# Performance work log

Measured on AMD Instinct MI355X. Metric: run time of the kernel, lower is better.

Reference implementation:

```python
import jax, jax.numpy as jnp
import numpy as np

B, S, T = 32, 64, 64          # batch, src_len, tgt_len
E, H, V = 512, 1024, 32000    # embed, hidden, vocab
WSCALE = 0.05                 # keep tanh/sigmoid in sane range


def setup_inputs() -> dict:
    key = jax.random.key(0)
    ks = jax.random.split(key, 14)
    n = lambda k, shp: jax.random.normal(k, shp, jnp.float32)
    return {
        "target": jax.random.randint(ks[0], (B, T), 0, V),
        "src_enc": n(ks[1], (B, S, 2 * H)),
        "h0": n(ks[2], (B, H)),
        "c0": n(ks[3], (B, H)),
        "emb": n(ks[4], (V, E)) * WSCALE,
        "W_ih": n(ks[5], (E, 4 * H)) * WSCALE,
        "W_hh": n(ks[6], (H, 4 * H)) * WSCALE,
        "b_rnn": jnp.zeros((4 * H,), jnp.float32),
        "W_attn": n(ks[7], (2 * H, H)) * WSCALE,
        "b_attn": jnp.zeros((H,), jnp.float32),
        "W_comb": n(ks[8], (2 * H, H)) * WSCALE,
        "b_comb": jnp.zeros((H,), jnp.float32),
        "W_out": n(ks[9], (H, V)) * WSCALE,
        "b_out": jnp.zeros((V,), jnp.float32),
    }


def reference(target, src_enc, h0, c0, emb, W_ih, W_hh, b_rnn,
              W_attn, b_attn, W_comb, b_comb, W_out, b_out):
    # Pre-project encoder states once (decode() applies attention.linear up front)
    enc_proj = src_enc @ W_attn + b_attn                 # [B,S,H]
    xs = emb[target[:, :-1]]                             # teacher forcing [B,T-1,E]
    xs = jnp.swapaxes(xs, 0, 1)                          # [T-1,B,E] for scan

    def step(carry, x_t):
        h, c = carry
        # LSTM cell (torch gate order i, f, g, o)
        gates = x_t @ W_ih + h @ W_hh + b_rnn            # [B,4H]
        i, f, g, o = jnp.split(gates, 4, axis=-1)
        c = jax.nn.sigmoid(f) * c + jax.nn.sigmoid(i) * jnp.tanh(g)
        h = jax.nn.sigmoid(o) * jnp.tanh(c)
        # Bilinear attention: score = h^T (W_attn e_s) over source positions
        scores = jnp.einsum('bsh,bh->bs', enc_proj, h)
        attn = jax.nn.softmax(scores, axis=-1)
        ctx = jnp.einsum('bs,bsh->bh', attn, enc_proj)   # [B,H]
        out = jnp.tanh(jnp.concatenate([h, ctx], axis=-1) @ W_comb + b_comb)
        return (h, c), out

    _, outs = jax.lax.scan(step, (h0, c0), xs)           # [T-1,B,H]
    outs = jnp.swapaxes(outs, 0, 1)                      # [B,T-1,H]
    logits = outs @ W_out + b_out                        # [B,T-1,V]
    return logits
```

## Files before the change

### kernel.cpp

```cpp
#include <hip/hip_runtime.h>
#include <stdint.h>

#define NB    32
#define NS    64
#define TDEC  63
#define NE    512
#define NH    1024
#define NV    32000

typedef float  floatx4 __attribute__((ext_vector_type(4)));
typedef short  short8  __attribute__((ext_vector_type(8)));
typedef short  short4v __attribute__((ext_vector_type(4)));

__device__ __forceinline__ float bf2f(short s) {
  return __uint_as_float(((uint32_t)(uint16_t)s) << 16);
}
__device__ __forceinline__ short f2bf(float f) {
  uint32_t u = __float_as_uint(f);
  uint32_t r = (u + 0x7fffu + ((u >> 16) & 1u)) >> 16;
  return (short)(uint16_t)r;
}
__device__ __forceinline__ float sigm(float x) { return 1.f / (1.f + expf(-x)); }

template<int PERM>
__global__ __launch_bounds__(256) void transpose_bf(
    const float* __restrict__ W, short* __restrict__ Wt, int K, int N)
{
  __shared__ float tile[32][33];
  int k0 = blockIdx.x * 32, n0 = blockIdx.y * 32;
  int tx = threadIdx.x & 31, ty = threadIdx.x >> 5;
#pragma unroll
  for (int r = 0; r < 32; r += 8)
    tile[ty + r][tx] = W[(size_t)(k0 + ty + r) * N + n0 + tx];
  __syncthreads();
  int kq = threadIdx.x & 7, nl = threadIdx.x >> 3;
  int n = n0 + nl;
  int rr = PERM ? ((n & 1023) * 4 + (n >> 10)) : n;
  short4v v;
#pragma unroll
  for (int q = 0; q < 4; ++q) v[q] = f2bf(tile[kq * 4 + q][nl]);
  *(short4v*)&Wt[(size_t)rr * K + k0 + kq * 4] = v;
}

template<int PERM>
__global__ __launch_bounds__(256) void transpose_bf_split(
    const float* __restrict__ W, short* __restrict__ Wt_hi,
    short* __restrict__ Wt_lo, int K, int N)
{
  __shared__ float tile[32][33];
  int k0 = blockIdx.x * 32, n0 = blockIdx.y * 32;
  int tx = threadIdx.x & 31, ty = threadIdx.x >> 5;
#pragma unroll
  for (int r = 0; r < 32; r += 8)
    tile[ty + r][tx] = W[(size_t)(k0 + ty + r) * N + n0 + tx];
  __syncthreads();
  int kq = threadIdx.x & 7, nl = threadIdx.x >> 3;
  int n = n0 + nl;
  int rr = PERM ? ((n & 1023) * 4 + (n >> 10)) : n;
  short4v vh, vl;
#pragma unroll
  for (int q = 0; q < 4; ++q) {
    float v = tile[kq * 4 + q][nl];
    short h = f2bf(v);
    vh[q] = h;
    vl[q] = f2bf(v - bf2f(h));
  }
  size_t o = (size_t)rr * K + k0 + kq * 4;
  *(short4v*)&Wt_hi[o] = vh;
  *(short4v*)&Wt_lo[o] = vl;
}

__global__ __launch_bounds__(256) void gather_init(
    const int* __restrict__ target, const float* __restrict__ emb,
    const float* __restrict__ h0, const float* __restrict__ c0,
    const float* __restrict__ brnn,
    short* __restrict__ xs, float* __restrict__ hf_ring,
    short* __restrict__ hhi_ring, short* __restrict__ hlo_ring,
    float* __restrict__ c_buf, float* __restrict__ brnn_p)
{
  const int NXS = TDEC * NB * NE;
  const int HN = NH * NB;
  int total = NXS + 2 * HN + 4096;
  for (int idx = blockIdx.x * 256 + threadIdx.x; idx < total; idx += gridDim.x * 256) {
    if (idx < NXS) {
      int row = idx >> 9, e = idx & 511;
      int t = row >> 5, b = row & 31;
      int token = target[b * 64 + t];
      xs[idx] = f2bf(emb[(size_t)token * NE + e]);
    } else if (idx < NXS + HN) {
      int r = idx - NXS;
      float v = h0[r];
      hf_ring[r] = v;
      short hh = f2bf(v);
      hhi_ring[r] = hh;
      hlo_ring[r] = f2bf(v - bf2f(hh));
    } else if (idx < NXS + 2 * HN) {
      int r = idx - NXS - HN;
      c_buf[r] = c0[r];
    } else {
      int c = idx - NXS - 2 * HN;
      brnn_p[c] = brnn[(c & 3) * 1024 + (c >> 2)];
    }
  }
}

template<int OUT_BF>
__global__ __launch_bounds__(256) void gemm_kernel(
    const short* __restrict__ Ab, const short* __restrict__ Bt,
    void* __restrict__ Cptr, const float* __restrict__ bias,
    int M, int N, int K)
{
  __shared__ short As[128 * 40];
  __shared__ short Bs[128 * 40];
  __shared__ float cst[OUT_BF ? 1 : 32 * 132];
  const int m0 = blockIdx.x * 128;
  const int n0 = blockIdx.y * 128;
  const int tid = threadIdx.x;
  const int lane = tid & 63;
  const int wid = tid >> 6;
  const int wr = wid >> 1, wc = wid & 1;

  floatx4 acc[4][4] = {};
  const int row = tid >> 1;
  const int kh  = (tid & 1) << 4;

  for (int k0 = 0; k0 < K; k0 += 32) {
    {
      int gm = m0 + row;
      short8 lo, hi;
      if (gm < M) {
        const short* src = Ab + (size_t)gm * K + k0 + kh;
        lo = *(const short8*)src;
        hi = *(const short8*)(src + 8);
      } else {
#pragma unroll
        for (int c = 0; c < 8; ++c) { lo[c] = 0; hi[c] = 0; }
      }
      *(short8*)&As[row * 40 + kh]     = lo;
      *(short8*)&As[row * 40 + kh + 8] = hi;
    }
    {
      const short* src = Bt + (size_t)(n0 + row) * K + k0 + kh;
      *(short8*)&Bs[row * 40 + kh]     = *(const short8*)src;
      *(short8*)&Bs[row * 40 + kh + 8] = *(const short8*)(src + 8);
    }
    __syncthreads();

    const int kA = (lane >> 4) << 3;
    const int rsel = lane & 15;
    short8 af[4], bfr[4];
#pragma unroll
    for (int mi = 0; mi < 4; ++mi)
      af[mi] = *(const short8*)&As[(wr * 64 + mi * 16 + rsel) * 40 + kA];
#pragma unroll
    for (int ni = 0; ni < 4; ++ni)
      bfr[ni] = *(const short8*)&Bs[(wc * 64 + ni * 16 + rsel) * 40 + kA];
#pragma unroll
    for (int mi = 0; mi < 4; ++mi)
#pragma unroll
      for (int ni = 0; ni < 4; ++ni)
        acc[mi][ni] = __builtin_amdgcn_mfma_f32_16x16x32_bf16(af[mi], bfr[ni], acc[mi][ni], 0, 0, 0);
    __syncthreads();
  }

  const int crow = (lane >> 4) * 4;
  const int ccol = lane & 15;
  if (OUT_BF) {
#pragma unroll
    for (int mi = 0; mi < 4; ++mi) {
#pragma unroll
      for (int ni = 0; ni < 4; ++ni) {
        int gn = n0 + wc * 64 + ni * 16 + ccol;
        float bv = bias[gn];
#pragma unroll
        for (int i = 0; i < 4; ++i) {
          int gm = m0 + wr * 64 + mi * 16 + crow + i;
          if (gm < M)
            ((short*)Cptr)[(size_t)gm * N + gn] = f2bf(acc[mi][ni][i] + bv);
        }
      }
    }
  } else {
#pragma unroll
    for (int p = 0; p < 4; ++p) {
      __syncthreads();
      if (wr == (p >> 1)) {
        int mi0 = (p & 1) * 2;
#pragma unroll
        for (int mm = 0; mm < 2; ++mm) {
#pragma unroll
          for (int ni = 0; ni < 4; ++ni) {
            int c = wc * 64 + ni * 16 + ccol;
#pragma unroll
            for (int i = 0; i < 4; ++i)
              cst[(mm * 16 + crow + i) * 132 + c] = acc[mi0 + mm][ni][i];
          }
        }
      }
      __syncthreads();
#pragma unroll
      for (int rep = 0; rep < 4; ++rep) {
        int cell = tid + rep * 256;
        int r = cell >> 5, q = cell & 31;
        int gm = m0 + p * 32 + r;
        int gn = n0 + q * 4;
        if (gm < M) {
          float4 bv = *(const float4*)&bias[gn];
          float4 v;
          v.x = cst[r * 132 + q * 4 + 0] + bv.x;
          v.y = cst[r * 132 + q * 4 + 1] + bv.y;
          v.z = cst[r * 132 + q * 4 + 2] + bv.z;
          v.w = cst[r * 132 + q * 4 + 3] + bv.w;
          *(float4*)&((float*)Cptr)[(size_t)gm * N + gn] = v;
        }
      }
    }
  }
}

__global__ __launch_bounds__(256) void gemm_split(
    const float* __restrict__ A, const short* __restrict__ Bt_hi,
    const short* __restrict__ Bt_lo, float* __restrict__ C,
    const float* __restrict__ bias, int M, int N, int K)
{
  __shared__ short As_hi[128 * 40];
  __shared__ short As_lo[128 * 40];
  __shared__ short Bs_hi[128 * 40];
  __shared__ short Bs_lo[128 * 40];
  const int m0 = blockIdx.x * 128;
  const int n0 = blockIdx.y * 128;
  const int tid = threadIdx.x;
  const int lane = tid & 63;
  const int wid = tid >> 6;
  const int wr = wid >> 1, wc = wid & 1;

  floatx4 acc[4][4] = {};
  const int row = tid >> 1;
  const int kh  = (tid & 1) << 4;

  for (int k0 = 0; k0 < K; k0 += 32) {
    {
      const float* src = A + (size_t)(m0 + row) * K + k0 + kh;
      short8 h0v, h1, l0, l1;
#pragma unroll
      for (int c = 0; c < 8; ++c) {
        float v = src[c];
        short h = f2bf(v); h0v[c] = h; l0[c] = f2bf(v - bf2f(h));
        float w = src[c + 8];
        short g = f2bf(w); h1[c] = g; l1[c] = f2bf(w - bf2f(g));
      }
      *(short8*)&As_hi[row * 40 + kh]     = h0v;
      *(short8*)&As_hi[row * 40 + kh + 8] = h1;
      *(short8*)&As_lo[row * 40 + kh]     = l0;
      *(short8*)&As_lo[row * 40 + kh + 8] = l1;
    }
    {
      size_t o = (size_t)(n0 + row) * K + k0 + kh;
      *(short8*)&Bs_hi[row * 40 + kh]     = *(const short8*)(Bt_hi + o);
      *(short8*)&Bs_hi[row * 40 + kh + 8] = *(const short8*)(Bt_hi + o + 8);
      *(short8*)&Bs_lo[row * 40 + kh]     = *(const short8*)(Bt_lo + o);
      *(short8*)&Bs_lo[row * 40 + kh + 8] = *(const short8*)(Bt_lo + o + 8);
    }
    __syncthreads();

    const int kA = (lane >> 4) << 3;
    const int rsel = lane & 15;
    short8 ah[4], al[4], bh[4], bl[4];
#pragma unroll
    for (int mi = 0; mi < 4; ++mi) {
      int off = (wr * 64 + mi * 16 + rsel) * 40 + kA;
      ah[mi] = *(const short8*)&As_hi[off];
      al[mi] = *(const short8*)&As_lo[off];
    }
#pragma unroll
    for (int ni = 0; ni < 4; ++ni) {
      int off = (wc * 64 + ni * 16 + rsel) * 40 + kA;
      bh[ni] = *(const short8*)&Bs_hi[off];
      bl[ni] = *(const short8*)&Bs_lo[off];
    }
#pragma unroll
    for (int mi = 0; mi < 4; ++mi)
#pragma unroll
      for (int ni = 0; ni < 4; ++ni) {
        floatx4 a = acc[mi][ni];
        a = __builtin_amdgcn_mfma_f32_16x16x32_bf16(al[mi], bh[ni], a, 0, 0, 0);
        a = __builtin_amdgcn_mfma_f32_16x16x32_bf16(ah[mi], bl[ni], a, 0, 0, 0);
        a = __builtin_amdgcn_mfma_f32_16x16x32_bf16(ah[mi], bh[ni], a, 0, 0, 0);
        acc[mi][ni] = a;
      }
    __syncthreads();
  }

  const int crow = (lane >> 4) * 4;
  const int ccol = lane & 15;
#pragma unroll
  for (int mi = 0; mi < 4; ++mi) {
#pragma unroll
    for (int ni = 0; ni < 4; ++ni) {
      int gn = n0 + wc * 64 + ni * 16 + ccol;
      float bv = bias[gn];
#pragma unroll
      for (int i = 0; i < 4; ++i) {
        int gm = m0 + wr * 64 + mi * 16 + crow + i;
        C[(size_t)gm * N + gn] = acc[mi][ni][i] + bv;
      }
    }
  }
}

__global__ __launch_bounds__(512) void scan_step(
    int iter,
    const short* __restrict__ Whp_hi,
    const short* __restrict__ Whp_lo,
    const short* __restrict__ WcT_hi,
    const short* __restrict__ WcT_lo,
    const float* __restrict__ bcomb,
    const float* __restrict__ encp,
    const short* __restrict__ gatesx,
    short* __restrict__ hhi_ring,
    short* __restrict__ hlo_ring,
    float* __restrict__ hf_ring,
    short* __restrict__ ctxhi_ring,
    short* __restrict__ ctxlo_ring,
    float* __restrict__ c_buf,
    short* __restrict__ outs)
{
  __shared__ float smem[8 * 32 * 33];
  const int blk = blockIdx.x;
  const int tid = threadIdx.x;
  const int lane = tid & 63;
  const int wid = tid >> 6;
  const int rsel = lane & 15;
  const int kA = (lane >> 4) * 8;
  const int crow = (lane >> 4) * 4;
  const int ccol = lane & 15;

  if (blk < 128) {
    const int t = iter;
    if (t >= TDEC) return;
    const size_t spv = (size_t)(t & 3) * (NH * NB);
    const size_t snw = (size_t)((t + 1) & 3) * (NH * NB);
    const short* Hh = hhi_ring + spv;
    const short* Hl = hlo_ring + spv;
    const int c0 = blk * 32;
    const int kb = wid * 128;

    floatx4 acc[2][2] = {};
    const short* wh0 = Whp_hi + (size_t)(c0 + rsel) * NH + kb + kA;
    const short* wl0 = Whp_lo + (size_t)(c0 + rsel) * NH + kb + kA;
    const short* wh1 = Whp_hi + (size_t)(c0 + 16 + rsel) * NH + kb + kA;
    const short* wl1 = Whp_lo + (size_t)(c0 + 16 + rsel) * NH + kb + kA;
    const short* ha0 = Hh + (size_t)rsel * NH + kb + kA;
    const short* la0 = Hl + (size_t)rsel * NH + kb + kA;
    const short* ha1 = Hh + (size_t)(16 + rsel) * NH + kb + kA;
    const short* la1 = Hl + (size_t)(16 + rsel) * NH + kb + kA;
#pragma unroll
    for (int kk = 0; kk < 4; ++kk) {
      int k0 = kk * 32;
      short8 a0h = *(const short8*)(ha0 + k0);
      short8 a0l = *(const short8*)(la0 + k0);
      short8 a1h = *(const short8*)(ha1 + k0);
      short8 a1l = *(const short8*)(la1 + k0);
      short8 b0h = *(const short8*)(wh0 + k0);
      short8 b0l = *(const short8*)(wl0 + k0);
      short8 b1h = *(const short8*)(wh1 + k0);
      short8 b1l = *(const short8*)(wl1 + k0);
      acc[0][0] = __builtin_amdgcn_mfma_f32_16x16x32_bf16(a0l, b0h, acc[0][0], 0, 0, 0);
      acc[0][0] = __builtin_amdgcn_mfma_f32_16x16x32_bf16(a0h, b0l, acc[0][0], 0, 0, 0);
      acc[0][0] = __builtin_amdgcn_mfma_f32_16x16x32_bf16(a0h, b0h, acc[0][0], 0, 0, 0);
      acc[0][1] = __builtin_amdgcn_mfma_f32_16x16x32_bf16(a0l, b1h, acc[0][1], 0, 0, 0);
      acc[0][1] = __builtin_amdgcn_mfma_f32_16x16x32_bf16(a0h, b1l, acc[0][1], 0, 0, 0);
      acc[0][1] = __builtin_amdgcn_mfma_f32_16x16x32_bf16(a0h, b1h, acc[0][1], 0, 0, 0);
      acc[1][0] = __builtin_amdgcn_mfma_f32_16x16x32_bf16(a1l, b0h, acc[1][0], 0, 0, 0);
      acc[1][0] = __builtin_amdgcn_mfma_f32_16x16x32_bf16(a1h, b0l, acc[1][0], 0, 0, 0);
      acc[1][0] = __builtin_amdgcn_mfma_f32_16x16x32_bf16(a1h, b0h, acc[1][0], 0, 0, 0);
      acc[1][1] = __builtin_amdgcn_mfma_f32_16x16x32_bf16(a1l, b1h, acc[1][1], 0, 0, 0);
      acc[1][1] = __builtin_amdgcn_mfma_f32_16x16x32_bf16(a1h, b1l, acc[1][1], 0, 0, 0);
      acc[1][1] = __builtin_amdgcn_mfma_f32_16x16x32_bf16(a1h, b1h, acc[1][1], 0, 0, 0);
    }
#pragma unroll
    for (int mi = 0; mi < 2; ++mi)
#pragma unroll
      for (int ni = 0; ni < 2; ++ni)
#pragma unroll
        for (int i = 0; i < 4; ++i)
          smem[wid * 1056 + (mi * 16 + crow + i) * 33 + ni * 16 + ccol] = acc[mi][ni][i];
    __syncthreads();
    if (tid < 256) {
      int b = tid & 31, jl = tid >> 5;
      float g[4];
#pragma unroll
      for (int q = 0; q < 4; ++q) {
        float s = 0;
#pragma unroll
        for (int w = 0; w < 8; ++w) s += smem[w * 1056 + b * 33 + jl * 4 + q];
        g[q] = s;
      }
      int jg = (c0 >> 2) + jl;
      const short* gx = gatesx + ((size_t)t * 32 + b) * 4096 + c0 + jl * 4;
      short4v gxv = *(const short4v*)gx;
      float gi = g[0] + bf2f(gxv[0]);
      float gf = g[1] + bf2f(gxv[1]);
      float gg = g[2] + bf2f(gxv[2]);
      float go = g[3] + bf2f(gxv[3]);
      float co = c_buf[b * NH + jg];
      float cn = sigm(gf) * co + sigm(gi) * tanhf(gg);
      float hn = sigm(go) * tanhf(cn);
      c_buf[b * NH + jg] = cn;
      hf_ring[snw + b * NH + jg] = hn;
      short hh = f2bf(hn);
      hhi_ring[snw + b * NH + jg] = hh;
      hlo_ring[snw + b * NH + jg] = f2bf(hn - bf2f(hh));
    }
  } else if (blk < 160) {
    const int t = iter - 1;
    if (t < 0 || t >= TDEC) return;
    const int b = blk - 128;
    const float* h = hf_ring + (size_t)((t + 1) & 3) * (NH * NB) + b * NH;
    const size_t cslot = (size_t)(t & 1) * (NH * NB) + b * NH;
    short* ctxh = ctxhi_ring + cslot;
    short* ctxl = ctxlo_ring + cslot;
    float* h_lds  = smem;
    float* sc_lds = smem + 1024;
    float* p_lds  = smem + 1088;
    if (tid < 256) {
      float4 v = ((const float4*)h)[tid];
      ((float4*)h_lds)[tid] = v;
    }
    __syncthreads();
    {
      const float4* hl4 = (const float4*)(h_lds + lane * 16);
      float4 hv0 = hl4[0], hv1 = hl4[1], hv2 = hl4[2], hv3 = hl4[3];
      for (int si = 0; si < 8; ++si) {
        int s = wid * 8 + si;
        const float4* ep = (const float4*)(encp + ((size_t)(b * 64 + s)) * NH + lane * 16);
        float4 e0 = ep[0], e1 = ep[1], e2 = ep[2], e3 = ep[3];
        float a = e0.x * hv0.x + e0.y * hv0.y + e0.z * hv0.z + e0.w * hv0.w;
        a = fmaf(e1.x, hv1.x, a); a = fmaf(e1.y, hv1.y, a);
        a = fmaf(e1.z, hv1.z, a); a = fmaf(e1.w, hv1.w, a);
        a = fmaf(e2.x, hv2.x, a); a = fmaf(e2.y, hv2.y, a);
        a = fmaf(e2.z, hv2.z, a); a = fmaf(e2.w, hv2.w, a);
        a = fmaf(e3.x, hv3.x, a); a = fmaf(e3.y, hv3.y, a);
        a = fmaf(e3.z, hv3.z, a); a = fmaf(e3.w, hv3.w, a);
#pragma unroll
        for (int off = 32; off; off >>= 1) a += __shfl_xor(a, off);
        if (lane == 0) sc_lds[s] = a;
      }
    }
    __syncthreads();
    if (tid < 64) {
      float sc = sc_lds[tid];
      float m = sc;
#pragma unroll
      for (int off = 32; off; off >>= 1) m = fmaxf(m, __shfl_xor(m, off));
      float e = expf(sc - m);
      float sum = e;
#pragma unroll
      for (int off = 32; off; off >>= 1) sum += __shfl_xor(sum, off);
      p_lds[tid] = e / sum;
    }
    __syncthreads();
    if (tid < 256) {
      int k4 = tid * 4;
      float a0 = 0, a1 = 0, a2 = 0, a3 = 0;
      const float* ep = encp + (size_t)(b * 64) * NH + k4;
      for (int s = 0; s < 64; ++s) {
        float p = p_lds[s];
        float4 e = *(const float4*)(ep + (size_t)s * NH);
        a0 = fmaf(p, e.x, a0); a1 = fmaf(p, e.y, a1);
        a2 = fmaf(p, e.z, a2); a3 = fmaf(p, e.w, a3);
      }
      short4v c4h, c4l;
      float av[4] = {a0, a1, a2, a3};
#pragma unroll
      for (int q = 0; q < 4; ++q) {
        short hh = f2bf(av[q]);
        c4h[q] = hh;
        c4l[q] = f2bf(av[q] - bf2f(hh));
      }
      *(short4v*)(ctxh + k4) = c4h;
      *(short4v*)(ctxl + k4) = c4l;
    }
  } else {
    const int t = iter - 2;
    if (t < 0) return;
    const int j0 = (blk - 160) * 16;
    const size_t hslot = (size_t)((t + 1) & 3) * (NH * NB);
    const size_t cslot = (size_t)(t & 1) * (NH * NB);
    const short* Ah = (wid < 4) ? (hhi_ring + hslot) : (ctxhi_ring + cslot);
    const short* Al = (wid < 4) ? (hlo_ring + hslot) : (ctxlo_ring + cslot);
    const int kb = (wid & 3) * 256;
    const int kabs = wid * 256;

    floatx4 acc[2] = {};
    const short* bhp = WcT_hi + (size_t)(j0 + rsel) * 2048 + kabs + kA;
    const short* blp = WcT_lo + (size_t)(j0 + rsel) * 2048 + kabs + kA;
    const short* a0hp = Ah + (size_t)rsel * NH + kb + kA;
    const short* a0lp = Al + (size_t)rsel * NH + kb + kA;
    const short* a1hp = Ah + (size_t)(16 + rsel) * NH + kb + kA;
    const short* a1lp = Al + (size_t)(16 + rsel) * NH + kb + kA;
#pragma unroll
    for (int kk = 0; kk < 8; ++kk) {
      int k0 = kk * 32;
      short8 a0h = *(const short8*)(a0hp + k0);
      short8 a0l = *(const short8*)(a0lp + k0);
      short8 a1h = *(const short8*)(a1hp + k0);
      short8 a1l = *(const short8*)(a1lp + k0);
      short8 b_h = *(const short8*)(bhp + k0);
      short8 b_l = *(const short8*)(blp + k0);
      acc[0] = __builtin_amdgcn_mfma_f32_16x16x32_bf16(a0l, b_h, acc[0], 0, 0, 0);
      acc[0] = __builtin_amdgcn_mfma_f32_16x16x32_bf16(a0h, b_l, acc[0], 0, 0, 0);
      acc[0] = __builtin_amdgcn_mfma_f32_16x16x32_bf16(a0h, b_h, acc[0], 0, 0, 0);
      acc[1] = __builtin_amdgcn_mfma_f32_16x16x32_bf16(a1l, b_h, acc[1], 0, 0, 0);
      acc[1] = __builtin_amdgcn_mfma_f32_16x16x32_bf16(a1h, b_l, acc[1], 0, 0, 0);
      acc[1] = __builtin_amdgcn_mfma_f32_16x16x32_bf16(a1h, b_h, acc[1], 0, 0, 0);
    }
#pragma unroll
    for (int mi = 0; mi < 2; ++mi)
#pragma unroll
      for (int i = 0; i < 4; ++i)
        smem[wid * 544 + (mi * 16 + crow + i) * 17 + ccol] = acc[mi][i];
    __syncthreads();
    {
      int b = tid & 31, jl = tid >> 5;
      float s = 0;
#pragma unroll
      for (int w = 0; w < 8; ++w) s += smem[w * 544 + b * 17 + jl];
      float v = tanhf(s + bcomb[j0 + jl]);
      outs[((size_t)b * TDEC + t) * NH + j0 + jl] = f2bf(v);
    }
  }
}

extern "C" void kernel_launch(void* const* d_in, const int* in_sizes, int n_in,
                              void* d_out, int out_size, void* d_ws, size_t ws_size,
                              hipStream_t stream)
{
  const int*   target = (const int*)  d_in[0];
  const float* src    = (const float*)d_in[1];
  const float* h0     = (const float*)d_in[2];
  const float* c0     = (const float*)d_in[3];
  const float* emb    = (const float*)d_in[4];
  const float* Wih    = (const float*)d_in[5];
  const float* Whh    = (const float*)d_in[6];
  const float* brnn   = (const float*)d_in[7];
  const float* Wattn  = (const float*)d_in[8];
  const float* battn  = (const float*)d_in[9];
  const float* Wcomb  = (const float*)d_in[10];
  const float* bcomb  = (const float*)d_in[11];
  const float* Wout   = (const float*)d_in[12];
  const float* bout   = (const float*)d_in[13];
  float* out = (float*)d_out;

  char* ws = (char*)d_ws;
  size_t off = 0;
  auto take = [&](size_t bytes) { char* p = ws + off; off += (bytes + 255) & ~(size_t)255; return p; };
  short* WoutT    = (short*)take((size_t)NV * NH * 2);
  short* WattnTh  = (short*)take((size_t)NH * 2048 * 2);
  short* WattnTl  = (short*)take((size_t)NH * 2048 * 2);
  short* WihTp    = (short*)take((size_t)4096 * NE * 2);
  short* WhpHi    = (short*)take((size_t)4096 * NH * 2);
  short* WhpLo    = (short*)take((size_t)4096 * NH * 2);
  short* WcTHi    = (short*)take((size_t)NH * 2048 * 2);
  short* WcTLo    = (short*)take((size_t)NH * 2048 * 2);
  short* xs_bf    = (short*)take((size_t)TDEC * NB * NE * 2);
  float* encp     = (float*)take((size_t)NB * NS * NH * 4);
  short* gatesx   = (short*)take((size_t)TDEC * NB * 4096 * 2);
  short* outs_bf  = (short*)take((size_t)TDEC * NB * NH * 2);
  short* hhi_ring = (short*)take((size_t)4 * NH * NB * 2);
  short* hlo_ring = (short*)take((size_t)4 * NH * NB * 2);
  float* hf_ring  = (float*)take((size_t)4 * NH * NB * 4);
  short* ctxhi_rg = (short*)take((size_t)2 * NH * NB * 2);
  short* ctxlo_rg = (short*)take((size_t)2 * NH * NB * 2);
  float* c_buf    = (float*)take((size_t)NH * NB * 4);
  float* brnn_p   = (float*)take((size_t)4096 * 4);
  if (off > ws_size) return;

  transpose_bf_split<0><<<dim3(2048 / 32, NH / 32), 256, 0, stream>>>(Wattn, WattnTh, WattnTl, 2048, NH);
  transpose_bf<1><<<dim3(NE / 32, 4096 / 32), 256, 0, stream>>>(Wih, WihTp, NE, 4096);
  transpose_bf_split<1><<<dim3(NH / 32, 4096 / 32), 256, 0, stream>>>(Whh, WhpHi, WhpLo, NH, 4096);
  transpose_bf_split<0><<<dim3(2048 / 32, NH / 32), 256, 0, stream>>>(Wcomb, WcTHi, WcTLo, 2048, NH);
  transpose_bf<0><<<dim3(NH / 32, NV / 32), 256, 0, stream>>>(Wout, WoutT, NH, NV);
  gather_init<<<1024, 256, 0, stream>>>(target, emb, h0, c0, brnn,
                                        xs_bf, hf_ring, hhi_ring, hlo_ring, c_buf, brnn_p);
  gemm_split<<<dim3(16, NH / 128), 256, 0, stream>>>(src, WattnTh, WattnTl, encp, battn, 2048, NH, 2048);
  gemm_kernel<1><<<dim3(16, 4096 / 128), 256, 0, stream>>>(xs_bf, WihTp, gatesx, brnn_p, TDEC * NB, 4096, NE);
  for (int i = 0; i < TDEC + 2; ++i)
    scan_step<<<224, 512, 0, stream>>>(i, WhpHi, WhpLo, WcTHi, WcTLo, bcomb, encp, gatesx,
                                       hhi_ring, hlo_ring, hf_ring, ctxhi_rg, ctxlo_rg,
                                       c_buf, outs_bf);
  gemm_kernel<0><<<dim3(16, NV / 128), 256, 0, stream>>>(outs_bf, WoutT, out, bout, TDEC * NB, NV, NH);
}
```

Measured before the change: 1.299 ms.

## Hoist attention and combine out of recurrence into batched kernels

Only the LSTM recurrence stays in the per-step launch loop. It now stores every hidden state in full-history buffers instead of a 4-slot ring. Attention for all timesteps then runs as one batched kernel, and the combine projection runs as one tiled split-bf16 GEMM over all rows, because neither depends on the recurrence. This shortens each sequential step and replaces many small per-step GEMVs with large parallel kernels, at the cost of larger workspace buffers and extra memory traffic for the stored states.

Result: no change. 1.282 ms (-1.3%).

```diff
diff --git a/kernel.cpp b/kernel.cpp
--- a/kernel.cpp
+++ b/kernel.cpp
@@ -74,8 +74,8 @@
     const int* __restrict__ target, const float* __restrict__ emb,
     const float* __restrict__ h0, const float* __restrict__ c0,
     const float* __restrict__ brnn,
-    short* __restrict__ xs, float* __restrict__ hf_ring,
-    short* __restrict__ hhi_ring, short* __restrict__ hlo_ring,
+    short* __restrict__ xs, float* __restrict__ hf_all,
+    short* __restrict__ hhi_all, short* __restrict__ hlo_all,
     float* __restrict__ c_buf, float* __restrict__ brnn_p)
 {
   const int NXS = TDEC * NB * NE;
@@ -90,10 +90,10 @@
     } else if (idx < NXS + HN) {
       int r = idx - NXS;
       float v = h0[r];
-      hf_ring[r] = v;
+      hf_all[r] = v;
       short hh = f2bf(v);
-      hhi_ring[r] = hh;
-      hlo_ring[r] = f2bf(v - bf2f(hh));
+      hhi_all[r] = hh;
+      hlo_all[r] = f2bf(v - bf2f(hh));
     } else if (idx < NXS + 2 * HN) {
       int r = idx - NXS - HN;
       c_buf[r] = c0[r];
@@ -308,22 +308,15 @@
   }
 }
 
-__global__ __launch_bounds__(512) void scan_step(
-    int iter,
+__global__ __launch_bounds__(512) void scan_a(
+    int t,
     const short* __restrict__ Whp_hi,
     const short* __restrict__ Whp_lo,
-    const short* __restrict__ WcT_hi,
-    const short* __restrict__ WcT_lo,
-    const float* __restrict__ bcomb,
-    const float* __restrict__ encp,
     const short* __restrict__ gatesx,
-    short* __restrict__ hhi_ring,
-    short* __restrict__ hlo_ring,
-    float* __restrict__ hf_ring,
-    short* __restrict__ ctxhi_ring,
-    short* __restrict__ ctxlo_ring,
-    float* __restrict__ c_buf,
-    short* __restrict__ outs)
+    short* __restrict__ hhi_all,
+    short* __restrict__ hlo_all,
+    float* __restrict__ hf_all,
+    float* __restrict__ c_buf)
 {
   __shared__ float smem[8 * 32 * 33];
   const int blk = blockIdx.x;
@@ -335,199 +328,255 @@
   const int crow = (lane >> 4) * 4;
   const int ccol = lane & 15;
 
-  if (blk < 128) {
-    const int t = iter;
-    if (t >= TDEC) return;
-    const size_t spv = (size_t)(t & 3) * (NH * NB);
-    const size_t snw = (size_t)((t + 1) & 3) * (NH * NB);
-    const short* Hh = hhi_ring + spv;
-    const short* Hl = hlo_ring + spv;
-    const int c0 = blk * 32;
-    const int kb = wid * 128;
-
-    floatx4 acc[2][2] = {};
-    const short* wh0 = Whp_hi + (size_t)(c0 + rsel) * NH + kb + kA;
-    const short* wl0 = Whp_lo + (size_t)(c0 + rsel) * NH + kb + kA;
-    const short* wh1 = Whp_hi + (size_t)(c0 + 16 + rsel) * NH + kb + kA;
-    const short* wl1 = Whp_lo + (size_t)(c0 + 16 + rsel) * NH + kb + kA;
-    const short* ha0 = Hh + (size_t)rsel * NH + kb + kA;
-    const short* la0 = Hl + (size_t)rsel * NH + kb + kA;
-    const short* ha1 = Hh + (size_t)(16 + rsel) * NH + kb + kA;
-    const short* la1 = Hl + (size_t)(16 + rsel) * NH + kb + kA;
-#pragma unroll
-    for (int kk = 0; kk < 4; ++kk) {
-      int k0 = kk * 32;
-      short8 a0h = *(const short8*)(ha0 + k0);
-      short8 a0l = *(const short8*)(la0 + k0);
-      short8 a1h = *(const short8*)(ha1 + k0);
-      short8 a1l = *(const short8*)(la1 + k0);
-      short8 b0h = *(const short8*)(wh0 + k0);
-      short8 b0l = *(const short8*)(wl0 + k0);
-      short8 b1h = *(const short8*)(wh1 + k0);
-      short8 b1l = *(const short8*)(wl1 + k0);
-      acc[0][0] = __builtin_amdgcn_mfma_f32_16x16x32_bf16(a0l, b0h, acc[0][0], 0, 0, 0);
-      acc[0][0] = __builtin_amdgcn_mfma_f32_16x16x32_bf16(a0h, b0l, acc[0][0], 0, 0, 0);
-      acc[0][0] = __builtin_amdgcn_mfma_f32_16x16x32_bf16(a0h, b0h, acc[0][0], 0, 0, 0);
-      acc[0][1] = __builtin_amdgcn_mfma_f32_16x16x32_bf16(a0l, b1h, acc[0][1], 0, 0, 0);
-      acc[0][1] = __builtin_amdgcn_mfma_f32_16x16x32_bf16(a0h, b1l, acc[0][1], 0, 0, 0);
-      acc[0][1] = __builtin_amdgcn_mfma_f32_16x16x32_bf16(a0h, b1h, acc[0][1], 0, 0, 0);
-      acc[1][0] = __builtin_amdgcn_mfma_f32_16x16x32_bf16(a1l, b0h, acc[1][0], 0, 0, 0);
-      acc[1][0] = __builtin_amdgcn_mfma_f32_16x16x32_bf16(a1h, b0l, acc[1][0], 0, 0, 0);
-      acc[1][0] = __builtin_amdgcn_mfma_f32_16x16x32_bf16(a1h, b0h, acc[1][0], 0, 0, 0);
-      acc[1][1] = __builtin_amdgcn_mfma_f32_16x16x32_bf16(a1l, b1h, acc[1][1], 0, 0, 0);
-      acc[1][1] = __builtin_amdgcn_mfma_f32_16x16x32_bf16(a1h, b1l, acc[1][1], 0, 0, 0);
-      acc[1][1] = __builtin_amdgcn_mfma_f32_16x16x32_bf16(a1h, b1h, acc[1][1], 0, 0, 0);
-    }
-#pragma unroll
-    for (int mi = 0; mi < 2; ++mi)
-#pragma unroll
-      for (int ni = 0; ni < 2; ++ni)
-#pragma unroll
-        for (int i = 0; i < 4; ++i)
-          smem[wid * 1056 + (mi * 16 + crow + i) * 33 + ni * 16 + ccol] = acc[mi][ni][i];
+  const size_t spv = (size_t)t * (NH * NB);
+  const size_t snw = (size_t)(t + 1) * (NH * NB);
+  const short* Hh = hhi_all + spv;
+  const short* Hl = hlo_all + spv;
+  const int c0 = blk * 32;
+  const int kb = wid * 128;
+
+  floatx4 acc[2][2] = {};
+  const short* wh0 = Whp_hi + (size_t)(c0 + rsel) * NH + kb + kA;
+  const short* wl0 = Whp_lo + (size_t)(c0 + rsel) * NH + kb + kA;
+  const short* wh1 = Whp_hi + (size_t)(c0 + 16 + rsel) * NH + kb + kA;
+  const short* wl1 = Whp_lo + (size_t)(c0 + 16 + rsel) * NH + kb + kA;
+  const short* ha0 = Hh + (size_t)rsel * NH + kb + kA;
+  const short* la0 = Hl + (size_t)rsel * NH + kb + kA;
+  const short* ha1 = Hh + (size_t)(16 + rsel) * NH + kb + kA;
+  const short* la1 = Hl + (size_t)(16 + rsel) * NH + kb + kA;
+#pragma unroll
+  for (int kk = 0; kk < 4; ++kk) {
+    int k0 = kk * 32;
+    short8 a0h = *(const short8*)(ha0 + k0);
+    short8 a0l = *(const short8*)(la0 + k0);
+    short8 a1h = *(const short8*)(ha1 + k0);
+    short8 a1l = *(const short8*)(la1 + k0);
+    short8 b0h = *(const short8*)(wh0 + k0);
+    short8 b0l = *(const short8*)(wl0 + k0);
+    short8 b1h = *(const short8*)(wh1 + k0);
+    short8 b1l = *(const short8*)(wl1 + k0);
+    acc[0][0] = __builtin_amdgcn_mfma_f32_16x16x32_bf16(a0l, b0h, acc[0][0], 0, 0, 0);
+    acc[0][0] = __builtin_amdgcn_mfma_f32_16x16x32_bf16(a0h, b0l, acc[0][0], 0, 0, 0);
+    acc[0][0] = __builtin_amdgcn_mfma_f32_16x16x32_bf16(a0h, b0h, acc[0][0], 0, 0, 0);
+    acc[0][1] = __builtin_amdgcn_mfma_f32_16x16x32_bf16(a0l, b1h, acc[0][1], 0, 0, 0);
+    acc[0][1] = __builtin_amdgcn_mfma_f32_16x16x32_bf16(a0h, b1l, acc[0][1], 0, 0, 0);
+    acc[0][1] = __builtin_amdgcn_mfma_f32_16x16x32_bf16(a0h, b1h, acc[0][1], 0, 0, 0);
+    acc[1][0] = __builtin_amdgcn_mfma_f32_16x16x32_bf16(a1l, b0h, acc[1][0], 0, 0, 0);
+    acc[1][0] = __builtin_amdgcn_mfma_f32_16x16x32_bf16(a1h, b0l, acc[1][0], 0, 0, 0);
+    acc[1][0] = __builtin_amdgcn_mfma_f32_16x16x32_bf16(a1h, b0h, acc[1][0], 0, 0, 0);
+    acc[1][1] = __builtin_amdgcn_mfma_f32_16x16x32_bf16(a1l, b1h, acc[1][1], 0, 0, 0);
+    acc[1][1] = __builtin_amdgcn_mfma_f32_16x16x32_bf16(a1h, b1l, acc[1][1], 0, 0, 0);
+    acc[1][1] = __builtin_amdgcn_mfma_f32_16x16x32_bf16(a1h, b1h, acc[1][1], 0, 0, 0);
+  }
+#pragma unroll
+  for (int mi = 0; mi < 2; ++mi)
+#pragma unroll
+    for (int ni = 0; ni < 2; ++ni)
+#pragma unroll
+      for (int i = 0; i < 4; ++i)
+        smem[wid * 1056 + (mi * 16 + crow + i) * 33 + ni * 16 + ccol] = acc[mi][ni][i];
+  __syncthreads();
+  if (tid < 256) {
+    int b = tid & 31, jl = tid >> 5;
+    float g[4];
+#pragma unroll
+    for (int q = 0; q < 4; ++q) {
+      float s = 0;
+#pragma unroll
+      for (int w = 0; w < 8; ++w) s += smem[w * 1056 + b * 33 + jl * 4 + q];
+      g[q] = s;
+    }
+    int jg = (c0 >> 2) + jl;
+    const short* gx = gatesx + ((size_t)t * 32 + b) * 4096 + c0 + jl * 4;
+    short4v gxv = *(const short4v*)gx;
+    float gi = g[0] + bf2f(gxv[0]);
+    float gf = g[1] + bf2f(gxv[1]);
+    float gg = g[2] + bf2f(gxv[2]);
+    float go = g[3] + bf2f(gxv[3]);
+    float co = c_buf[b * NH + jg];
+    float cn = sigm(gf) * co + sigm(gi) * tanhf(gg);
+    float hn = sigm(go) * tanhf(cn);
+    c_buf[b * NH + jg] = cn;
+    hf_all[snw + b * NH + jg] = hn;
+    short hh = f2bf(hn);
+    hhi_all[snw + b * NH + jg] = hh;
+    hlo_all[snw + b * NH + jg] = f2bf(hn - bf2f(hh));
+  }
+}
+
+__global__ __launch_bounds__(256) void attn_batch(
+    const float* __restrict__ encp,
+    const float* __restrict__ hf_all,
+    short* __restrict__ ctxhi_all,
+    short* __restrict__ ctxlo_all)
+{
+  __shared__ float h_lds[NH];
+  __shared__ float part[4 * 64];
+  __shared__ float sc_lds[64];
+  __shared__ float p_lds[64];
+  const int blk = blockIdx.x;
+  const int b = blk / TDEC;
+  const int t = blk % TDEC;
+  const int tid = threadIdx.x;
+  const float* h = hf_all + ((size_t)(t + 1) * 32 + b) * NH;
+
+  ((float4*)h_lds)[tid] = ((const float4*)h)[tid];
+  __syncthreads();
+  {
+    int s = tid & 63, kc = tid >> 6;
+    const float4* ep = (const float4*)(encp + ((size_t)(b * 64 + s)) * NH + kc * 256);
+    const float4* hp = (const float4*)(h_lds + kc * 256);
+    float ac0 = 0, ac1 = 0, ac2 = 0, ac3 = 0;
+#pragma unroll
+    for (int i = 0; i < 64; i += 4) {
+      float4 e0 = ep[i],     h0v = hp[i];
+      float4 e1 = ep[i + 1], h1v = hp[i + 1];
+      float4 e2 = ep[i + 2], h2v = hp[i + 2];
+      float4 e3 = ep[i + 3], h3v = hp[i + 3];
+      ac0 = fmaf(e0.x, h0v.x, ac0); ac0 = fmaf(e0.y, h0v.y, ac0);
+      ac0 = fmaf(e0.z, h0v.z, ac0); ac0 = fmaf(e0.w, h0v.w, ac0);
+      ac1 = fmaf(e1.x, h1v.x, ac1); ac1 = fmaf(e1.y, h1v.y, ac1);
+      ac1 = fmaf(e1.z, h1v.z, ac1); ac1 = fmaf(e1.w, h1v.w, ac1);
+      ac2 = fmaf(e2.x, h2v.x, ac2); ac2 = fmaf(e2.y, h2v.y, ac2);
+      ac2 = fmaf(e2.z, h2v.z, ac2); ac2 = fmaf(e2.w, h2v.w, ac2);
+      ac3 = fmaf(e3.x, h3v.x, ac3); ac3 = fmaf(e3.y, h3v.y, ac3);
+      ac3 = fmaf(e3.z, h3v.z, ac3); ac3 = fmaf(e3.w, h3v.w, ac3);
+    }
+    part[kc * 64 + s] = (ac0 + ac1) + (ac2 + ac3);
+  }
+  __syncthreads();
+  if (tid < 64) {
+    float sc = part[tid] + part[64 + tid] + part[128 + tid] + part[192 + tid];
+    sc_lds[tid] = sc;
+    float m = sc;
+#pragma unroll
+    for (int off = 32; off; off >>= 1) m = fmaxf(m, __shfl_xor(m, off));
+    float e = expf(sc - m);
+    float sum = e;
+#pragma unroll
+    for (int off = 32; off; off >>= 1) sum += __shfl_xor(sum, off);
+    p_lds[tid] = e / sum;
+  }
+  __syncthreads();
+  {
+    int k4 = tid * 4;
+    float a0 = 0, a1 = 0, a2 = 0, a3 = 0;
+    const float* ep = encp + (size_t)(b * 64) * NH + k4;
+    for (int s = 0; s < 64; ++s) {
+      float p = p_lds[s];
+      float4 e = *(const float4*)(ep + (size_t)s * NH);
+      a0 = fmaf(p, e.x, a0); a1 = fmaf(p, e.y, a1);
+      a2 = fmaf(p, e.z, a2); a3 = fmaf(p, e.w, a3);
+    }
+    size_t crow = ((size_t)t * 32 + b) * NH + k4;
+    short4v c4h, c4l;
+    float av[4] = {a0, a1, a2, a3};
+#pragma unroll
+    for (int q = 0; q < 4; ++q) {
+      short hh = f2bf(av[q]);
+      c4h[q] = hh;
+      c4l[q] = f2bf(av[q] - bf2f(hh));
+    }
+    *(short4v*)(ctxhi_all + crow) = c4h;
+    *(short4v*)(ctxlo_all + crow) = c4l;
+  }
+}
+
+__global__ __launch_bounds__(256) void gemm_comb(
+    const short* __restrict__ Ah_hi,
+    const short* __restrict__ Ah_lo,
+    const short* __restrict__ Cx_hi,
+    const short* __restrict__ Cx_lo,
+    const short* __restrict__ Bt_hi,
+    const short* __restrict__ Bt_lo,
+    const float* __restrict__ bcomb,
+    short* __restrict__ outs)
+{
+  __shared__ short As_hi[128 * 40];
+  __shared__ short As_lo[128 * 40];
+  __shared__ short Bs_hi[128 * 40];
+  __shared__ short Bs_lo[128 * 40];
+  const int m0 = blockIdx.x * 128;
+  const int n0 = blockIdx.y * 128;
+  const int tid = threadIdx.x;
+  const int lane = tid & 63;
+  const int wid = tid >> 6;
+  const int wr = wid >> 1, wc = wid & 1;
+
+  floatx4 acc[4][4] = {};
+  const int row = tid >> 1;
+  const int kh  = (tid & 1) << 4;
+
+  for (int k0 = 0; k0 < 2048; k0 += 32) {
+    {
+      int gr = m0 + row;
+      const short* sh;
+      const short* sl;
+      if (k0 < NH) {
+        sh = Ah_hi + (size_t)gr * NH + k0 + kh;
+        sl = Ah_lo + (size_t)gr * NH + k0 + kh;
+      } else {
+        sh = Cx_hi + (size_t)gr * NH + (k0 - NH) + kh;
+        sl = Cx_lo + (size_t)gr * NH + (k0 - NH) + kh;
+      }
+      *(short8*)&As_hi[row * 40 + kh]     = *(const short8*)sh;
+      *(short8*)&As_hi[row * 40 + kh + 8] = *(const short8*)(sh + 8);
+      *(short8*)&As_lo[row * 40 + kh]     = *(const short8*)sl;
+      *(short8*)&As_lo[row * 40 + kh + 8] = *(const short8*)(sl + 8);
+    }
+    {
+      size_t o = (size_t)(n0 + row) * 2048 + k0 + kh;
+      *(short8*)&Bs_hi[row * 40 + kh]     = *(const short8*)(Bt_hi + o);
+      *(short8*)&Bs_hi[row * 40 + kh + 8] = *(const short8*)(Bt_hi + o + 8);
+      *(short8*)&Bs_lo[row * 40 + kh]     = *(const short8*)(Bt_lo + o);
+      *(short8*)&Bs_lo[row * 40 + kh + 8] = *(const short8*)(Bt_lo + o + 8);
+    }
     __syncthreads();
-    if (tid < 256) {
-      int b = tid & 31, jl = tid >> 5;
-      float g[4];
-#pragma unroll
-      for (int q = 0; q < 4; ++q) {
-        float s = 0;
-#pragma unroll
-        for (int w = 0; w < 8; ++w) s += smem[w * 1056 + b * 33 + jl * 4 + q];
-        g[q] = s;
-      }
-      int jg = (c0 >> 2) + jl;
-      const short* gx = gatesx + ((size_t)t * 32 + b) * 4096 + c0 + jl * 4;
-      short4v gxv = *(const short4v*)gx;
-      float gi = g[0] + bf2f(gxv[0]);
-      float gf = g[1] + bf2f(gxv[1]);
-      float gg = g[2] + bf2f(gxv[2]);
-      float go = g[3] + bf2f(gxv[3]);
-      float co = c_buf[b * NH + jg];
-      float cn = sigm(gf) * co + sigm(gi) * tanhf(gg);
-      float hn = sigm(go) * tanhf(cn);
-      c_buf[b * NH + jg] = cn;
-      hf_ring[snw + b * NH + jg] = hn;
-      short hh = f2bf(hn);
-      hhi_ring[snw + b * NH + jg] = hh;
-      hlo_ring[snw + b * NH + jg] = f2bf(hn - bf2f(hh));
-    }
-  } else if (blk < 160) {
-    const int t = iter - 1;
-    if (t < 0 || t >= TDEC) return;
-    const int b = blk - 128;
-    const float* h = hf_ring + (size_t)((t + 1) & 3) * (NH * NB) + b * NH;
-    const size_t cslot = (size_t)(t & 1) * (NH * NB) + b * NH;
-    short* ctxh = ctxhi_ring + cslot;
-    short* ctxl = ctxlo_ring + cslot;
-    float* h_lds  = smem;
-    float* sc_lds = smem + 1024;
-    float* p_lds  = smem + 1088;
-    if (tid < 256) {
-      float4 v = ((const float4*)h)[tid];
-      ((float4*)h_lds)[tid] = v;
-    }
+
+    const int kA = (lane >> 4) << 3;
+    const int rsel = lane & 15;
+    short8 ah[4], al[4], bh[4], bl[4];
+#pragma unroll
+    for (int mi = 0; mi < 4; ++mi) {
+      int off = (wr * 64 + mi * 16 + rsel) * 40 + kA;
+      ah[mi] = *(const short8*)&As_hi[off];
+      al[mi] = *(const short8*)&As_lo[off];
+    }
+#pragma unroll
+    for (int ni = 0; ni < 4; ++ni) {
+      int off = (wc * 64 + ni * 16 + rsel) * 40 + kA;
+      bh[ni] = *(const short8*)&Bs_hi[off];
+      bl[ni] = *(const short8*)&Bs_lo[off];
+    }
+#pragma unroll
+    for (int mi = 0; mi < 4; ++mi)
+#pragma unroll
+      for (int ni = 0; ni < 4; ++ni) {
+        floatx4 a = acc[mi][ni];
+        a = __builtin_amdgcn_mfma_f32_16x16x32_bf16(al[mi], bh[ni], a, 0, 0, 0);
+        a = __builtin_amdgcn_mfma_f32_16x16x32_bf16(ah[mi], bl[ni], a, 0, 0, 0);
+        a = __builtin_amdgcn_mfma_f32_16x16x32_bf16(ah[mi], bh[ni], a, 0, 0, 0);
+        acc[mi][ni] = a;
+      }
     __syncthreads();
-    {
-      const float4* hl4 = (const float4*)(h_lds + lane * 16);
-      float4 hv0 = hl4[0], hv1 = hl4[1], hv2 = hl4[2], hv3 = hl4[3];
-      for (int si = 0; si < 8; ++si) {
-        int s = wid * 8 + si;
-        const float4* ep = (const float4*)(encp + ((size_t)(b * 64 + s)) * NH + lane * 16);
-        float4 e0 = ep[0], e1 = ep[1], e2 = ep[2], e3 = ep[3];
-        float a = e0.x * hv0.x + e0.y * hv0.y + e0.z * hv0.z + e0.w * hv0.w;
-        a = fmaf(e1.x, hv1.x, a); a = fmaf(e1.y, hv1.y, a);
-        a = fmaf(e1.z, hv1.z, a); a = fmaf(e1.w, hv1.w, a);
-        a = fmaf(e2.x, hv2.x, a); a = fmaf(e2.y, hv2.y, a);
-        a = fmaf(e2.z, hv2.z, a); a = fmaf(e2.w, hv2.w, a);
-        a = fmaf(e3.x, hv3.x, a); a = fmaf(e3.y, hv3.y, a);
-        a = fmaf(e3.z, hv3.z, a); a = fmaf(e3.w, hv3.w, a);
-#pragma unroll
-        for (int off = 32; off; off >>= 1) a += __shfl_xor(a, off);
-        if (lane == 0) sc_lds[s] = a;
-      }
-    }
-    __syncthreads();
-    if (tid < 64) {
-      float sc = sc_lds[tid];
-      float m = sc;
-#pragma unroll
-      for (int off = 32; off; off >>= 1) m = fmaxf(m, __shfl_xor(m, off));
-      float e = expf(sc - m);
-      float sum = e;
-#pragma unroll
-      for (int off = 32; off; off >>= 1) sum += __shfl_xor(sum, off);
-      p_lds[tid] = e / sum;
-    }
-    __syncthreads();
-    if (tid < 256) {
-      int k4 = tid * 4;
-      float a0 = 0, a1 = 0, a2 = 0, a3 = 0;
-      const float* ep = encp + (size_t)(b * 64) * NH + k4;
-      for (int s = 0; s < 64; ++s) {
-        float p = p_lds[s];
-        float4 e = *(const float4*)(ep + (size_t)s * NH);
-        a0 = fmaf(p, e.x, a0); a1 = fmaf(p, e.y, a1);
-        a2 = fmaf(p, e.z, a2); a3 = fmaf(p, e.w, a3);
-      }
-      short4v c4h, c4l;
-      float av[4] = {a0, a1, a2, a3};
-#pragma unroll
-      for (int q = 0; q < 4; ++q) {
-        short hh = f2bf(av[q]);
-        c4h[q] = hh;
-        c4l[q] = f2bf(av[q] - bf2f(hh));
-      }
-      *(short4v*)(ctxh + k4) = c4h;
-      *(short4v*)(ctxl + k4) = c4l;
-    }
-  } else {
-    const int t = iter - 2;
-    if (t < 0) return;
-    const int j0 = (blk - 160) * 16;
-    const size_t hslot = (size_t)((t + 1) & 3) * (NH * NB);
-    const size_t cslot = (size_t)(t & 1) * (NH * NB);
-    const short* Ah = (wid < 4) ? (hhi_ring + hslot) : (ctxhi_ring + cslot);
-    const short* Al = (wid < 4) ? (hlo_ring + hslot) : (ctxlo_ring + cslot);
-    const int kb = (wid & 3) * 256;
-    const int kabs = wid * 256;
-
-    floatx4 acc[2] = {};
-    const short* bhp = WcT_hi + (size_t)(j0 + rsel) * 2048 + kabs + kA;
-    const short* blp = WcT_lo + (size_t)(j0 + rsel) * 2048 + kabs + kA;
-    const short* a0hp = Ah + (size_t)rsel * NH + kb + kA;
-    const short* a0lp = Al + (size_t)rsel * NH + kb + kA;
-    const short* a1hp = Ah + (size_t)(16 + rsel) * NH + kb + kA;
-    const short* a1lp = Al + (size_t)(16 + rsel) * NH + kb + kA;
-#pragma unroll
-    for (int kk = 0; kk < 8; ++kk) {
-      int k0 = kk * 32;
-      short8 a0h = *(const short8*)(a0hp + k0);
-      short8 a0l = *(const short8*)(a0lp + k0);
-      short8 a1h = *(const short8*)(a1hp + k0);
-      short8 a1l = *(const short8*)(a1lp + k0);
-      short8 b_h = *(const short8*)(bhp + k0);
-      short8 b_l = *(const short8*)(blp + k0);
-      acc[0] = __builtin_amdgcn_mfma_f32_16x16x32_bf16(a0l, b_h, acc[0], 0, 0, 0);
-      acc[0] = __builtin_amdgcn_mfma_f32_16x16x32_bf16(a0h, b_l, acc[0], 0, 0, 0);
-      acc[0] = __builtin_amdgcn_mfma_f32_16x16x32_bf16(a0h, b_h, acc[0], 0, 0, 0);
-      acc[1] = __builtin_amdgcn_mfma_f32_16x16x32_bf16(a1l, b_h, acc[1], 0, 0, 0);
-      acc[1] = __builtin_amdgcn_mfma_f32_16x16x32_bf16(a1h, b_l, acc[1], 0, 0, 0);
-      acc[1] = __builtin_amdgcn_mfma_f32_16x16x32_bf16(a1h, b_h, acc[1], 0, 0, 0);
-    }
-#pragma unroll
-    for (int mi = 0; mi < 2; ++mi)
-#pragma unroll
-      for (int i = 0; i < 4; ++i)
-        smem[wid * 544 + (mi * 16 + crow + i) * 17 + ccol] = acc[mi][i];
-    __syncthreads();
-    {
-      int b = tid & 31, jl = tid >> 5;
-      float s = 0;
-#pragma unroll
-      for (int w = 0; w < 8; ++w) s += smem[w * 544 + b * 17 + jl];
-      float v = tanhf(s + bcomb[j0 + jl]);
-      outs[((size_t)b * TDEC + t) * NH + j0 + jl] = f2bf(v);
+  }
+
+  const int crow = (lane >> 4) * 4;
+  const int ccol = lane & 15;
+#pragma unroll
+  for (int mi = 0; mi < 4; ++mi) {
+#pragma unroll
+    for (int ni = 0; ni < 4; ++ni) {
+      int gn = n0 + wc * 64 + ni * 16 + ccol;
+      float bv = bcomb[gn];
+#pragma unroll
+      for (int i = 0; i < 4; ++i) {
+        int gm = m0 + wr * 64 + mi * 16 + crow + i;
+        if (gm < TDEC * NB) {
+          int tt = gm >> 5, bb = gm & 31;
+          outs[((size_t)bb * TDEC + tt) * NH + gn] = f2bf(tanhf(acc[mi][ni][i] + bv));
+        }
+      }
     }
   }
 }
@@ -567,11 +616,11 @@
   float* encp     = (float*)take((size_t)NB * NS * NH * 4);
   short* gatesx   = (short*)take((size_t)TDEC * NB * 4096 * 2);
   short* outs_bf  = (short*)take((size_t)TDEC * NB * NH * 2);
-  short* hhi_ring = (short*)take((size_t)4 * NH * NB * 2);
-  short* hlo_ring = (short*)take((size_t)4 * NH * NB * 2);
-  float* hf_ring  = (float*)take((size_t)4 * NH * NB * 4);
-  short* ctxhi_rg = (short*)take((size_t)2 * NH * NB * 2);
-  short* ctxlo_rg = (short*)take((size_t)2 * NH * NB * 2);
+  float* hf_all   = (float*)take((size_t)65 * NB * NH * 4);
+  short* hhi_all  = (short*)take((size_t)65 * NB * NH * 2);
+  short* hlo_all  = (short*)take((size_t)65 * NB * NH * 2);
+  short* ctxhi_a  = (short*)take((size_t)2048 * NH * 2);
+  short* ctxlo_a  = (short*)take((size_t)2048 * NH * 2);
   float* c_buf    = (float*)take((size_t)NH * NB * 4);
   float* brnn_p   = (float*)take((size_t)4096 * 4);
   if (off > ws_size) return;
@@ -582,12 +631,13 @@
   transpose_bf_split<0><<<dim3(2048 / 32, NH / 32), 256, 0, stream>>>(Wcomb, WcTHi, WcTLo, 2048, NH);
   transpose_bf<0><<<dim3(NH / 32, NV / 32), 256, 0, stream>>>(Wout, WoutT, NH, NV);
   gather_init<<<1024, 256, 0, stream>>>(target, emb, h0, c0, brnn,
-                                        xs_bf, hf_ring, hhi_ring, hlo_ring, c_buf, brnn_p);
+                                        xs_bf, hf_all, hhi_all, hlo_all, c_buf, brnn_p);
   gemm_split<<<dim3(16, NH / 128), 256, 0, stream>>>(src, WattnTh, WattnTl, encp, battn, 2048, NH, 2048);
   gemm_kernel<1><<<dim3(16, 4096 / 128), 256, 0, stream>>>(xs_bf, WihTp, gatesx, brnn_p, TDEC * NB, 4096, NE);
-  for (int i = 0; i < TDEC + 2; ++i)
-    scan_step<<<224, 512, 0, stream>>>(i, WhpHi, WhpLo, WcTHi, WcTLo, bcomb, encp, gatesx,
-                                       hhi_ring, hlo_ring, hf_ring, ctxhi_rg, ctxlo_rg,
-                                       c_buf, outs_bf);
+  for (int t = 0; t < TDEC; ++t)
+    scan_a<<<128, 512, 0, stream>>>(t, WhpHi, WhpLo, gatesx, hhi_all, hlo_all, hf_all, c_buf);
+  attn_batch<<<TDEC * NB, 256, 0, stream>>>(encp, hf_all, ctxhi_a, ctxlo_a);
+  gemm_comb<<<dim3(16, 8), 256, 0, stream>>>(hhi_all + (size_t)32 * NH, hlo_all + (size_t)32 * NH,
+                                             ctxhi_a, ctxlo_a, WcTHi, WcTLo, bcomb, outs_bf);
   gemm_kernel<0><<<dim3(16, NV / 128), 256, 0, stream>>>(outs_bf, WoutT, out, bout, TDEC * NB, NV, NH);
 }
```
